# Optimization experiments

Measured on AMD Instinct MI355X. Metric: run time of the kernel, lower is better.

Reference implementation:

```python
import jax, jax.numpy as jnp
import numpy as np

N_NODES = 100_000
N_EDGES = 3_200_000


def setup_inputs() -> dict:
    key = jax.random.key(0)
    k = jax.random.split(key, 7)
    x = jax.random.normal(k[0], (N_NODES, 1), dtype=jnp.float32)
    edge_index = jax.random.randint(k[1], (2, N_EDGES), 0, N_NODES, dtype=jnp.int64)
    edge_weight = jax.random.uniform(k[2], (N_EDGES,), dtype=jnp.float32)
    # GCNConv params (glorot-style scale)
    W1 = jax.random.normal(k[3], (1, 16), dtype=jnp.float32) * 0.5
    b1 = jnp.zeros((16,), dtype=jnp.float32)
    W2 = jax.random.normal(k[4], (16, 2), dtype=jnp.float32) * 0.25
    b2 = jnp.zeros((2,), dtype=jnp.float32)
    return {"x": x, "edge_index": edge_index, "edge_weight": edge_weight,
            "W1": W1, "b1": b1, "W2": W2, "b2": b2}


def reference(x, edge_index, edge_weight, W1, b1, W2, b2):
    N = x.shape[0]
    src, dst = edge_index[0], edge_index[1]
    # GCN normalization with self-loops (fill value 1.0), cached across both layers
    loop = jnp.arange(N, dtype=edge_index.dtype)
    src_f = jnp.concatenate([src, loop])            # [E+N]
    dst_f = jnp.concatenate([dst, loop])            # [E+N]
    w_f = jnp.concatenate([edge_weight, jnp.ones((N,), dtype=edge_weight.dtype)])
    deg = jax.ops.segment_sum(w_f, dst_f, num_segments=N)   # [N]
    dinv = jnp.where(deg > 0, jax.lax.rsqrt(deg), 0.0)
    norm = dinv[src_f] * w_f * dinv[dst_f]          # [E+N]

    def gcn_layer(h, W, b):
        h = h @ W                                   # [N, F_out]
        msg = norm[:, None] * h[src_f]              # gather + weight  [E+N, F_out]
        agg = jax.ops.segment_sum(msg, dst_f, num_segments=N)  # scatter-add [N, F_out]
        return agg + b

    h = jax.nn.relu(gcn_layer(x, W1, b1))
    # F.dropout(training=self.training): identity at inference (reference is eval mode)
    out = gcn_layer(h, W2, b2)
    return jax.nn.log_softmax(out, axis=1)
```

## Files before the change

### kernel.cpp

```cpp
#include <hip/hip_runtime.h>
#include <math.h>


static constexpr int BLOCK_S   = 512;
static constexpr int EPB       = 4096;
static constexpr int VITERS    = EPB / (BLOCK_S * 4);
static constexpr int CHUNK     = 128;
static constexpr int LOG_CHUNK = 7;
static constexpr int BLOCK_A   = 512;
static constexpr int MAXNB     = 1024;
static constexpr int MAXBLK    = 1024;
static constexpr int TABCAP    = 5120;

__device__ __forceinline__ unsigned int incl_scan512(unsigned int v,
                                                     unsigned int* wsum, int t) {
    unsigned int x = v;
#pragma unroll
    for (int off = 1; off < 64; off <<= 1) {
        unsigned int y = __shfl_up(x, off, 64);
        if ((t & 63) >= off) x += y;
    }
    if ((t & 63) == 63) wsum[t >> 6] = x;
    __syncthreads();
    if (t < 8) {
        unsigned int s = wsum[t];
#pragma unroll
        for (int off = 1; off < 8; off <<= 1) {
            unsigned int y = __shfl_up(s, off, 64);
            if (t >= off) s += y;
        }
        wsum[t] = s;
    }
    __syncthreads();
    return x + ((t >= 64) ? wsum[(t >> 6) - 1] : 0u);
}

__device__ __forceinline__ int run_adj_fallback(const unsigned int* cumx,
                                                const int* radj,
                                                unsigned int i, int nblk) {
    int lo = 0, hi = nblk - 1;
    while (lo < hi) {
        int mid = (lo + hi + 1) >> 1;
        if (cumx[mid] <= i) lo = mid; else hi = mid - 1;
    }
    return radj[lo];
}


__global__ __launch_bounds__(BLOCK_S) void scatter_kernel(
    const int* __restrict__ src, const int* __restrict__ dst,
    const float* __restrict__ w,
    unsigned int* __restrict__ rowOffT,
    unsigned long long* __restrict__ payload,
    int E, int nb, int nblk) {
    __shared__ unsigned long long pbuf[EPB];
    __shared__ unsigned int hist[MAXNB];
    __shared__ unsigned int wsum[8];
    const int blk  = blockIdx.x;
    const int base = blk * EPB;
    const int nE   = min(EPB, E - base);
    const int t    = threadIdx.x;

    hist[t]           = 0u;
    hist[t + BLOCK_S] = 0u;
    __syncthreads();

    int4 dc[VITERS];
#pragma unroll
    for (int i = 0; i < VITERS; ++i) {
        const int k = 4 * t + i * 4 * BLOCK_S;
        int4 d4 = make_int4(0, 0, 0, 0);
        if (k < nE) {
            d4 = *reinterpret_cast<const int4*>(&dst[base + k]);
            atomicAdd(&hist[(unsigned int)d4.x >> LOG_CHUNK], 1u);
            atomicAdd(&hist[(unsigned int)d4.y >> LOG_CHUNK], 1u);
            atomicAdd(&hist[(unsigned int)d4.z >> LOG_CHUNK], 1u);
            atomicAdd(&hist[(unsigned int)d4.w >> LOG_CHUNK], 1u);
        }
        dc[i] = d4;
    }
    __syncthreads();

    const unsigned int v0 = hist[2 * t], v1 = hist[2 * t + 1];
    const unsigned int pr = v0 + v1;
    const unsigned int inclp = incl_scan512(pr, wsum, t);
    const unsigned int ex0 = inclp - pr;
    const unsigned int ex1 = ex0 + v0;
    if (2 * t < nb)     rowOffT[(size_t)(2 * t) * nblk + blk]     = ex0;
    if (2 * t + 1 < nb) rowOffT[(size_t)(2 * t + 1) * nblk + blk] = ex1;
    if (t == 0)         rowOffT[(size_t)nb * nblk + blk] = (unsigned int)nE;
    hist[2 * t]     = ex0;
    hist[2 * t + 1] = ex1;
    __syncthreads();

#pragma unroll
    for (int i = 0; i < VITERS; ++i) {
        const int k = 4 * t + i * 4 * BLOCK_S;
        if (k < nE) {
            const int4   d4 = dc[i];
            const int4   s4 = *reinterpret_cast<const int4*>(&src[base + k]);
            const float4 w4 = *reinterpret_cast<const float4*>(&w[base + k]);
#define SCAT_ONE(dd, ss, ww)                                                  \
            {                                                                 \
                const unsigned int slot =                                     \
                    atomicAdd(&hist[(unsigned int)(dd) >> LOG_CHUNK], 1u);    \
                pbuf[slot] =                                                  \
                    ((unsigned long long)__float_as_uint(ww) << 32) |         \
                    ((unsigned int)(ss) << LOG_CHUNK) |                       \
                    (unsigned int)((dd) & (CHUNK - 1));                       \
            }
            SCAT_ONE(d4.x, s4.x, w4.x)
            SCAT_ONE(d4.y, s4.y, w4.y)
            SCAT_ONE(d4.z, s4.z, w4.z)
            SCAT_ONE(d4.w, s4.w, w4.w)
#undef SCAT_ONE
        }
    }
    __syncthreads();
    for (int k2 = t; k2 < (nE >> 1); k2 += BLOCK_S) {
        ulonglong2 v = *reinterpret_cast<const ulonglong2*>(&pbuf[2 * k2]);
        *reinterpret_cast<ulonglong2*>(&payload[(size_t)base + 2 * k2]) = v;
    }
}


#define AGG_PROLOGUE                                                          \
    const int b = blockIdx.x, t = threadIdx.x;                                \
    const int e0 = 2 * t, e1 = 2 * t + 1;                                     \
    unsigned int s00 = 0, s01 = 0, len0 = 0, len1 = 0;                        \
    if (e0 < nblk) {                                                          \
        const uint2 r0 =                                                      \
            *reinterpret_cast<const uint2*>(&rowOffT[(size_t)b * nblk + e0]); \
        const uint2 r1 =                                                      \
            *reinterpret_cast<const uint2*>(&rowOffT[(size_t)(b + 1) * nblk + e0]); \
        s00 = r0.x; s01 = r0.y;                                               \
        len0 = r1.x - r0.x;                                                   \
        len1 = (e1 < nblk) ? (r1.y - r0.y) : 0u;                              \
    }                                                                         \
    const unsigned int pr_    = len0 + len1;                                  \
    const unsigned int inclp_ = incl_scan512(pr_, wsum, t);                   \
    const unsigned int ex0_   = inclp_ - pr_;                                 \
    const unsigned int ex1_   = ex0_ + len0;                                  \
    if (e0 < nblk) { cumx[e0] = ex0_; radj[e0] = (int)s00 - (int)ex0_ + e0 * EPB; } \
    if (e1 < nblk) { cumx[e1] = ex1_; radj[e1] = (int)s01 - (int)ex1_ + e1 * EPB; } \
    if (t == ((nblk - 1) >> 1)) totsh = inclp_;                               \
    if (t < CHUNK) acc[t] = 0.0f;                                             \
    __syncthreads();                                                          \
    const unsigned int total = totsh;                                         \
    for (int r = e0; r <= e1 && r < nblk; ++r) {                              \
        const unsigned int beg = cumx[r];                                     \
        const unsigned int end = (r == nblk - 1) ? total : cumx[r + 1];       \
        const unsigned int lim = min(end, (unsigned int)TABCAP);              \
        const int a_ = radj[r];                                               \
        for (unsigned int i = beg; i < lim; ++i) table[i] = a_;               \
    }                                                                         \
    __syncthreads();

#define TAB(i) (((i) < (unsigned int)TABCAP) ? table[i]                       \
                                             : run_adj_fallback(cumx, radj, (i), nblk))

__global__ __launch_bounds__(BLOCK_A) void deg_dinv_kernel(
    const unsigned long long* __restrict__ payload,
    const unsigned int* __restrict__ rowOffT,
    const float* __restrict__ x,
    float* __restrict__ dinv, float* __restrict__ xd,
    int N, int nb, int nblk) {
    __shared__ unsigned int cumx[MAXBLK];
    __shared__ int          radj[MAXBLK];
    __shared__ float        acc[CHUNK];
    __shared__ int          table[TABCAP];
    __shared__ unsigned int wsum[8];
    __shared__ unsigned int totsh;
    AGG_PROLOGUE
    unsigned int i = t;
    for (; i + 3u * BLOCK_A < total; i += 4u * BLOCK_A) {
        const unsigned int i0 = i, i1 = i + BLOCK_A, i2 = i + 2u * BLOCK_A,
                           i3 = i + 3u * BLOCK_A;
        const int a0 = TAB(i0), a1 = TAB(i1), a2 = TAB(i2), a3 = TAB(i3);
        const unsigned long long p0 = payload[(unsigned int)(a0 + (int)i0)];
        const unsigned long long p1 = payload[(unsigned int)(a1 + (int)i1)];
        const unsigned long long p2 = payload[(unsigned int)(a2 + (int)i2)];
        const unsigned long long p3 = payload[(unsigned int)(a3 + (int)i3)];
        atomicAdd(&acc[(unsigned int)p0 & (CHUNK - 1)],
                  __uint_as_float((unsigned int)(p0 >> 32)));
        atomicAdd(&acc[(unsigned int)p1 & (CHUNK - 1)],
                  __uint_as_float((unsigned int)(p1 >> 32)));
        atomicAdd(&acc[(unsigned int)p2 & (CHUNK - 1)],
                  __uint_as_float((unsigned int)(p2 >> 32)));
        atomicAdd(&acc[(unsigned int)p3 & (CHUNK - 1)],
                  __uint_as_float((unsigned int)(p3 >> 32)));
    }
    for (; i < total; i += BLOCK_A) {
        const int adj = TAB(i);
        const unsigned long long p = payload[(unsigned int)(adj + (int)i)];
        atomicAdd(&acc[(unsigned int)p & (CHUNK - 1)],
                  __uint_as_float((unsigned int)(p >> 32)));
    }
    __syncthreads();
    const int n = b * CHUNK + t;
    if (t < CHUNK && n < N) {
        const float d = acc[t] + 1.0f;
        const float r = (d > 0.0f) ? rsqrtf(d) : 0.0f;
        dinv[n] = r;
        xd[n]   = r * x[n];
    }
}

__global__ __launch_bounds__(BLOCK_A) void s_gamma_kernel(
    const unsigned long long* __restrict__ payload,
    const unsigned int* __restrict__ rowOffT,
    const float* __restrict__ dinv,
    const float* __restrict__ xd,
    const float* __restrict__ W1,
    const float* __restrict__ b1,
    const float* __restrict__ W2,
    float* __restrict__ gd, int N, int nb, int nblk) {
    __shared__ unsigned int cumx[MAXBLK];
    __shared__ int          radj[MAXBLK];
    __shared__ float        acc[CHUNK];
    __shared__ int          table[TABCAP];
    __shared__ unsigned int wsum[8];
    __shared__ unsigned int totsh;
    AGG_PROLOGUE
    unsigned int i = t;
    for (; i + 3u * BLOCK_A < total; i += 4u * BLOCK_A) {
        const unsigned int i0 = i, i1 = i + BLOCK_A, i2 = i + 2u * BLOCK_A,
                           i3 = i + 3u * BLOCK_A;
        const int a0 = TAB(i0), a1 = TAB(i1), a2 = TAB(i2), a3 = TAB(i3);
        const unsigned long long p0 = payload[(unsigned int)(a0 + (int)i0)];
        const unsigned long long p1 = payload[(unsigned int)(a1 + (int)i1)];
        const unsigned long long p2 = payload[(unsigned int)(a2 + (int)i2)];
        const unsigned long long p3 = payload[(unsigned int)(a3 + (int)i3)];
        const float f0 = xd[(int)(((unsigned int)p0) >> LOG_CHUNK)];
        const float f1 = xd[(int)(((unsigned int)p1) >> LOG_CHUNK)];
        const float f2 = xd[(int)(((unsigned int)p2) >> LOG_CHUNK)];
        const float f3 = xd[(int)(((unsigned int)p3) >> LOG_CHUNK)];
        atomicAdd(&acc[(unsigned int)p0 & (CHUNK - 1)],
                  __uint_as_float((unsigned int)(p0 >> 32)) * f0);
        atomicAdd(&acc[(unsigned int)p1 & (CHUNK - 1)],
                  __uint_as_float((unsigned int)(p1 >> 32)) * f1);
        atomicAdd(&acc[(unsigned int)p2 & (CHUNK - 1)],
                  __uint_as_float((unsigned int)(p2 >> 32)) * f2);
        atomicAdd(&acc[(unsigned int)p3 & (CHUNK - 1)],
                  __uint_as_float((unsigned int)(p3 >> 32)) * f3);
    }
    for (; i < total; i += BLOCK_A) {
        const int adj = TAB(i);
        const unsigned long long p = payload[(unsigned int)(adj + (int)i)];
        atomicAdd(&acc[(unsigned int)p & (CHUNK - 1)],
                  __uint_as_float((unsigned int)(p >> 32)) *
                      xd[(int)(((unsigned int)p) >> LOG_CHUNK)]);
    }
    __syncthreads();
    const int n = b * CHUNK + t;
    if (t < CHUNK && n < N) {
        const float dv = dinv[n];
        const float sv = dv * (acc[t] + xd[n]);
        float g = 0.0f;
#pragma unroll
        for (int f = 0; f < 16; ++f) {
            const float h = fmaxf(sv * W1[f] + b1[f], 0.0f);
            g += h * (W2[2 * f + 1] - W2[2 * f + 0]);
        }
        gd[n] = dv * g;
    }
}

__global__ __launch_bounds__(BLOCK_A) void d_out_kernel(
    const unsigned long long* __restrict__ payload,
    const unsigned int* __restrict__ rowOffT,
    const float* __restrict__ dinv,
    const float* __restrict__ gd,
    const float* __restrict__ b2,
    float* __restrict__ out, int N, int nb, int nblk) {
    __shared__ unsigned int cumx[MAXBLK];
    __shared__ int          radj[MAXBLK];
    __shared__ float        acc[CHUNK];
    __shared__ int          table[TABCAP];
    __shared__ unsigned int wsum[8];
    __shared__ unsigned int totsh;
    AGG_PROLOGUE
    unsigned int i = t;
    for (; i + 3u * BLOCK_A < total; i += 4u * BLOCK_A) {
        const unsigned int i0 = i, i1 = i + BLOCK_A, i2 = i + 2u * BLOCK_A,
                           i3 = i + 3u * BLOCK_A;
        const int a0 = TAB(i0), a1 = TAB(i1), a2 = TAB(i2), a3 = TAB(i3);
        const unsigned long long p0 = payload[(unsigned int)(a0 + (int)i0)];
        const unsigned long long p1 = payload[(unsigned int)(a1 + (int)i1)];
        const unsigned long long p2 = payload[(unsigned int)(a2 + (int)i2)];
        const unsigned long long p3 = payload[(unsigned int)(a3 + (int)i3)];
        const float f0 = gd[(int)(((unsigned int)p0) >> LOG_CHUNK)];
        const float f1 = gd[(int)(((unsigned int)p1) >> LOG_CHUNK)];
        const float f2 = gd[(int)(((unsigned int)p2) >> LOG_CHUNK)];
        const float f3 = gd[(int)(((unsigned int)p3) >> LOG_CHUNK)];
        atomicAdd(&acc[(unsigned int)p0 & (CHUNK - 1)],
                  __uint_as_float((unsigned int)(p0 >> 32)) * f0);
        atomicAdd(&acc[(unsigned int)p1 & (CHUNK - 1)],
                  __uint_as_float((unsigned int)(p1 >> 32)) * f1);
        atomicAdd(&acc[(unsigned int)p2 & (CHUNK - 1)],
                  __uint_as_float((unsigned int)(p2 >> 32)) * f2);
        atomicAdd(&acc[(unsigned int)p3 & (CHUNK - 1)],
                  __uint_as_float((unsigned int)(p3 >> 32)) * f3);
    }
    for (; i < total; i += BLOCK_A) {
        const int adj = TAB(i);
        const unsigned long long p = payload[(unsigned int)(adj + (int)i)];
        atomicAdd(&acc[(unsigned int)p & (CHUNK - 1)],
                  __uint_as_float((unsigned int)(p >> 32)) *
                      gd[(int)(((unsigned int)p) >> LOG_CHUNK)]);
    }
    __syncthreads();
    const int n = b * CHUNK + t;
    if (t < CHUNK && n < N) {
        const float dv = dinv[n];
        const float d = dv * (acc[t] + gd[n]) + (b2[1] - b2[0]);
        const float lse = fmaxf(d, 0.0f) + log1pf(expf(-fabsf(d)));
        out[2 * n + 0] = -lse;
        out[2 * n + 1] = d - lse;
    }
}


static constexpr int BLOCK = 256;

__global__ void zero_kernel(float* __restrict__ a, float* __restrict__ b, int n2) {
    int i = blockIdx.x * blockDim.x + threadIdx.x;
    if (i < n2) { a[i] = 0.0f; b[i] = 0.0f; }
}
__global__ void deg_kernel(const int* __restrict__ dst, const float* __restrict__ w,
                           float* __restrict__ deg, int E) {
    int e = blockIdx.x * blockDim.x + threadIdx.x;
    if (e < E) atomicAdd(&deg[dst[e]], w[e]);
}
__global__ void dinv_kernel(float* __restrict__ deg, int N) {
    int n = blockIdx.x * blockDim.x + threadIdx.x;
    if (n < N) {
        float d = deg[n] + 1.0f;
        deg[n] = (d > 0.0f) ? rsqrtf(d) : 0.0f;
    }
}
__global__ void s_kernel(const int* __restrict__ src, const int* __restrict__ dst,
                         const float* __restrict__ w, const float* __restrict__ dinv,
                         const float* __restrict__ x, float* __restrict__ s, int E) {
    int e = blockIdx.x * blockDim.x + threadIdx.x;
    if (e < E) {
        int si = src[e], di = dst[e];
        atomicAdd(&s[di], dinv[si] * w[e] * dinv[di] * x[si]);
    }
}
__global__ void g_kernel(const float* __restrict__ s, const float* __restrict__ dinv,
                         const float* __restrict__ x, const float* __restrict__ W1,
                         const float* __restrict__ b1, const float* __restrict__ W2,
                         float2* __restrict__ g, int N) {
    int n = blockIdx.x * blockDim.x + threadIdx.x;
    if (n < N) {
        float dv = dinv[n];
        float sv = s[n] + dv * dv * x[n];
        float g0 = 0.0f, g1 = 0.0f;
#pragma unroll
        for (int f = 0; f < 16; ++f) {
            float h = fmaxf(sv * W1[f] + b1[f], 0.0f);
            g0 += h * W2[2 * f + 0];
            g1 += h * W2[2 * f + 1];
        }
        g[n] = make_float2(g0, g1);
    }
}
__global__ void agg2_kernel(const int* __restrict__ src, const int* __restrict__ dst,
                            const float* __restrict__ w, const float* __restrict__ dinv,
                            const float2* __restrict__ g, float* __restrict__ agg, int E) {
    int e = blockIdx.x * blockDim.x + threadIdx.x;
    if (e < E) {
        int si = src[e], di = dst[e];
        float norm = dinv[si] * w[e] * dinv[di];
        float2 gv = g[si];
        atomicAdd(&agg[2 * di + 0], norm * gv.x);
        atomicAdd(&agg[2 * di + 1], norm * gv.y);
    }
}
__global__ void out_kernel(float* __restrict__ out, const float* __restrict__ dinv,
                           const float2* __restrict__ g, const float* __restrict__ b2, int N) {
    int n = blockIdx.x * blockDim.x + threadIdx.x;
    if (n < N) {
        float dv2 = dinv[n] * dinv[n];
        float2 gv = g[n];
        float a0 = out[2 * n + 0] + dv2 * gv.x + b2[0];
        float a1 = out[2 * n + 1] + dv2 * gv.y + b2[1];
        float m = fmaxf(a0, a1);
        float lse = m + logf(expf(a0 - m) + expf(a1 - m));
        out[2 * n + 0] = a0 - lse;
        out[2 * n + 1] = a1 - lse;
    }
}


extern "C" void kernel_launch(void* const* d_in, const int* in_sizes, int n_in,
                              void* d_out, int out_size, void* d_ws, size_t ws_size,
                              hipStream_t stream) {
    const float* x  = (const float*)d_in[0];
    const int*   ei = (const int*)d_in[1];
    const float* w  = (const float*)d_in[2];
    const float* W1 = (const float*)d_in[3];
    const float* b1 = (const float*)d_in[4];
    const float* W2 = (const float*)d_in[5];
    const float* b2 = (const float*)d_in[6];
    float* out = (float*)d_out;

    const int N = in_sizes[0];
    const int E = in_sizes[2];
    const int* src = ei;
    const int* dst = ei + E;

    const int nb   = (N + CHUNK - 1) / CHUNK;
    const int nblk = (E + EPB - 1) / EPB;

    size_t off = 0;
    size_t payload_off = off;  off += (size_t)nblk * EPB * 8;
    size_t rowoff_off  = off;  off += (size_t)(nb + 1) * nblk * 4 + 8;
    off = (off + 7) & ~(size_t)7;
    size_t dinv_off    = off;  off += (size_t)N * 4;
    size_t xd_off      = off;  off += (size_t)N * 4;
    size_t gd_off      = off;  off += (size_t)N * 4;
    const size_t required = off;

    const bool fits = (nb <= MAXNB && nb <= 2 * BLOCK_S && nblk <= MAXBLK &&
                       nblk <= 2 * BLOCK_A && (nblk & 1) == 0 && (E % 4) == 0 &&
                       ws_size >= required);

    if (fits) {
        char* wsb = (char*)d_ws;
        unsigned long long* payload = (unsigned long long*)(wsb + payload_off);
        unsigned int* rowOffT = (unsigned int*)(wsb + rowoff_off);
        float* dinv = (float*)(wsb + dinv_off);
        float* xd   = (float*)(wsb + xd_off);
        float* gd   = (float*)(wsb + gd_off);

        scatter_kernel <<<nblk, BLOCK_S, 0, stream>>>(src, dst, w, rowOffT, payload,
                                                      E, nb, nblk);
        deg_dinv_kernel<<<nb, BLOCK_A, 0, stream>>>(payload, rowOffT, x,
                                                    dinv, xd, N, nb, nblk);
        s_gamma_kernel <<<nb, BLOCK_A, 0, stream>>>(payload, rowOffT, dinv, xd,
                                                    W1, b1, W2, gd, N, nb, nblk);
        d_out_kernel   <<<nb, BLOCK_A, 0, stream>>>(payload, rowOffT, dinv, gd, b2,
                                                    out, N, nb, nblk);
    } else {
        float*  ws   = (float*)d_ws;
        float*  dinv = ws;
        float*  s    = ws + (size_t)N;
        float2* g    = (float2*)(ws + (size_t)2 * N);
        const int gridE  = (E + BLOCK - 1) / BLOCK;
        const int gridN  = (N + BLOCK - 1) / BLOCK;
        const int gridN2 = (2 * N + BLOCK - 1) / BLOCK;
        zero_kernel<<<gridN2, BLOCK, 0, stream>>>(ws, out, 2 * N);
        deg_kernel <<<gridE,  BLOCK, 0, stream>>>(dst, w, dinv, E);
        dinv_kernel<<<gridN,  BLOCK, 0, stream>>>(dinv, N);
        s_kernel   <<<gridE,  BLOCK, 0, stream>>>(src, dst, w, dinv, x, s, E);
        g_kernel   <<<gridN,  BLOCK, 0, stream>>>(s, dinv, x, W1, b1, W2, g, N);
        agg2_kernel<<<gridE,  BLOCK, 0, stream>>>(src, dst, w, dinv, g, out, E);
        out_kernel <<<gridN,  BLOCK, 0, stream>>>(out, dinv, g, b2, N);
    }
}
```

Before: 188.5 us.

## Compact per-bucket edge payload in degree pass for contiguous reuse in later aggregations

The degree kernel now copies each bucket's edge records, which it already reads from the segmented payload, into a contiguous padded per-bucket buffer and records the bucket count. The two later aggregation kernels read that compact buffer with 16-byte vector loads. This skips their run-offset scan, table build and indirect segmented addressing. Buckets larger than the pad size fall back to the old path through a sentinel count. The trade-off is an extra write of the payload in the first pass and more workspace memory.

```diff
diff --git a/kernel.cpp b/kernel.cpp
--- a/kernel.cpp
+++ b/kernel.cpp
@@ -11,6 +11,8 @@
 static constexpr int MAXNB     = 1024;
 static constexpr int MAXBLK    = 1024;
 static constexpr int TABCAP    = 5120;
+static constexpr int PAD       = 5120;
+static constexpr unsigned int SENT = 0xFFFFFFFFu;
 
 __device__ __forceinline__ unsigned int incl_scan512(unsigned int v,
                                                      unsigned int* wsum, int t) {
@@ -125,34 +127,34 @@
 
 
 #define AGG_PROLOGUE                                                          \
-    const int b = blockIdx.x, t = threadIdx.x;                                \
-    const int e0 = 2 * t, e1 = 2 * t + 1;                                     \
     unsigned int s00 = 0, s01 = 0, len0 = 0, len1 = 0;                        \
-    if (e0 < nblk) {                                                          \
-        const uint2 r0 =                                                      \
-            *reinterpret_cast<const uint2*>(&rowOffT[(size_t)b * nblk + e0]); \
-        const uint2 r1 =                                                      \
-            *reinterpret_cast<const uint2*>(&rowOffT[(size_t)(b + 1) * nblk + e0]); \
-        s00 = r0.x; s01 = r0.y;                                               \
-        len0 = r1.x - r0.x;                                                   \
-        len1 = (e1 < nblk) ? (r1.y - r0.y) : 0u;                              \
-    }                                                                         \
-    const unsigned int pr_    = len0 + len1;                                  \
-    const unsigned int inclp_ = incl_scan512(pr_, wsum, t);                   \
-    const unsigned int ex0_   = inclp_ - pr_;                                 \
-    const unsigned int ex1_   = ex0_ + len0;                                  \
-    if (e0 < nblk) { cumx[e0] = ex0_; radj[e0] = (int)s00 - (int)ex0_ + e0 * EPB; } \
-    if (e1 < nblk) { cumx[e1] = ex1_; radj[e1] = (int)s01 - (int)ex1_ + e1 * EPB; } \
-    if (t == ((nblk - 1) >> 1)) totsh = inclp_;                               \
-    if (t < CHUNK) acc[t] = 0.0f;                                             \
-    __syncthreads();                                                          \
-    const unsigned int total = totsh;                                         \
-    for (int r = e0; r <= e1 && r < nblk; ++r) {                              \
-        const unsigned int beg = cumx[r];                                     \
-        const unsigned int end = (r == nblk - 1) ? total : cumx[r + 1];       \
-        const unsigned int lim = min(end, (unsigned int)TABCAP);              \
-        const int a_ = radj[r];                                               \
-        for (unsigned int i = beg; i < lim; ++i) table[i] = a_;               \
+    {                                                                         \
+        const int e0 = 2 * t, e1 = 2 * t + 1;                                 \
+        if (e0 < nblk) {                                                      \
+            const uint2 r0 =                                                  \
+                *reinterpret_cast<const uint2*>(&rowOffT[(size_t)b * nblk + e0]); \
+            const uint2 r1 =                                                  \
+                *reinterpret_cast<const uint2*>(&rowOffT[(size_t)(b + 1) * nblk + e0]); \
+            s00 = r0.x; s01 = r0.y;                                           \
+            len0 = r1.x - r0.x;                                               \
+            len1 = (e1 < nblk) ? (r1.y - r0.y) : 0u;                          \
+        }                                                                     \
+        const unsigned int pr_    = len0 + len1;                              \
+        const unsigned int inclp_ = incl_scan512(pr_, wsum, t);               \
+        const unsigned int ex0_   = inclp_ - pr_;                             \
+        const unsigned int ex1_   = ex0_ + len0;                              \
+        if (e0 < nblk) { cumx[e0] = ex0_; radj[e0] = (int)s00 - (int)ex0_ + e0 * EPB; } \
+        if (e1 < nblk) { cumx[e1] = ex1_; radj[e1] = (int)s01 - (int)ex1_ + e1 * EPB; } \
+        if (t == ((nblk - 1) >> 1)) totsh = inclp_;                           \
+        __syncthreads();                                                      \
+        const unsigned int total_ = totsh;                                    \
+        for (int r = e0; r <= e1 && r < nblk; ++r) {                          \
+            const unsigned int beg = cumx[r];                                 \
+            const unsigned int end = (r == nblk - 1) ? total_ : cumx[r + 1];  \
+            const unsigned int lim = min(end, (unsigned int)TABCAP);          \
+            const int a_ = radj[r];                                           \
+            for (unsigned int i = beg; i < lim; ++i) table[i] = a_;           \
+        }                                                                     \
     }                                                                         \
     __syncthreads();
 
@@ -161,6 +163,8 @@
 
 __global__ __launch_bounds__(BLOCK_A) void deg_dinv_kernel(
     const unsigned long long* __restrict__ payload,
+    unsigned long long* __restrict__ payload2,
+    unsigned int* __restrict__ bucketCnt,
     const unsigned int* __restrict__ rowOffT,
     const float* __restrict__ x,
     float* __restrict__ dinv, float* __restrict__ xd,
@@ -171,7 +175,13 @@
     __shared__ int          table[TABCAP];
     __shared__ unsigned int wsum[8];
     __shared__ unsigned int totsh;
+    const int b = blockIdx.x, t = threadIdx.x;
+    if (t < CHUNK) acc[t] = 0.0f;
     AGG_PROLOGUE
+    const unsigned int total = totsh;
+    const bool canw = (total <= (unsigned int)PAD);
+    if (t == 0) bucketCnt[b] = canw ? total : SENT;
+    unsigned long long* const p2 = payload2 + (size_t)b * PAD;
     unsigned int i = t;
     for (; i + 3u * BLOCK_A < total; i += 4u * BLOCK_A) {
         const unsigned int i0 = i, i1 = i + BLOCK_A, i2 = i + 2u * BLOCK_A,
@@ -179,20 +189,24 @@
         const int a0 = TAB(i0), a1 = TAB(i1), a2 = TAB(i2), a3 = TAB(i3);
         const unsigned long long p0 = payload[(unsigned int)(a0 + (int)i0)];
         const unsigned long long p1 = payload[(unsigned int)(a1 + (int)i1)];
-        const unsigned long long p2 = payload[(unsigned int)(a2 + (int)i2)];
+        const unsigned long long p2v = payload[(unsigned int)(a2 + (int)i2)];
         const unsigned long long p3 = payload[(unsigned int)(a3 + (int)i3)];
+        if (canw) {
+            p2[i0] = p0; p2[i1] = p1; p2[i2] = p2v; p2[i3] = p3;
+        }
         atomicAdd(&acc[(unsigned int)p0 & (CHUNK - 1)],
                   __uint_as_float((unsigned int)(p0 >> 32)));
         atomicAdd(&acc[(unsigned int)p1 & (CHUNK - 1)],
                   __uint_as_float((unsigned int)(p1 >> 32)));
-        atomicAdd(&acc[(unsigned int)p2 & (CHUNK - 1)],
-                  __uint_as_float((unsigned int)(p2 >> 32)));
+        atomicAdd(&acc[(unsigned int)p2v & (CHUNK - 1)],
+                  __uint_as_float((unsigned int)(p2v >> 32)));
         atomicAdd(&acc[(unsigned int)p3 & (CHUNK - 1)],
                   __uint_as_float((unsigned int)(p3 >> 32)));
     }
     for (; i < total; i += BLOCK_A) {
         const int adj = TAB(i);
         const unsigned long long p = payload[(unsigned int)(adj + (int)i)];
+        if (canw) p2[i] = p;
         atomicAdd(&acc[(unsigned int)p & (CHUNK - 1)],
                   __uint_as_float((unsigned int)(p >> 32)));
     }
@@ -206,8 +220,62 @@
     }
 }
 
+
+#define FAST_BODY(GATHER_ARR)                                                 \
+    const size_t gbase = (size_t)b * PAD;                                     \
+    const unsigned int npair = cnt >> 1;                                      \
+    unsigned int j = t;                                                       \
+    for (; j + 3u * BLOCK_A < npair; j += 4u * BLOCK_A) {                     \
+        const ulonglong2 q0 = *reinterpret_cast<const ulonglong2*>(&payload2[gbase + 2u * j]); \
+        const ulonglong2 q1 = *reinterpret_cast<const ulonglong2*>(&payload2[gbase + 2u * (j + BLOCK_A)]); \
+        const ulonglong2 q2 = *reinterpret_cast<const ulonglong2*>(&payload2[gbase + 2u * (j + 2u * BLOCK_A)]); \
+        const ulonglong2 q3 = *reinterpret_cast<const ulonglong2*>(&payload2[gbase + 2u * (j + 3u * BLOCK_A)]); \
+        const float f0a = GATHER_ARR[(int)(((unsigned int)q0.x) >> LOG_CHUNK)]; \
+        const float f0b = GATHER_ARR[(int)(((unsigned int)q0.y) >> LOG_CHUNK)]; \
+        const float f1a = GATHER_ARR[(int)(((unsigned int)q1.x) >> LOG_CHUNK)]; \
+        const float f1b = GATHER_ARR[(int)(((unsigned int)q1.y) >> LOG_CHUNK)]; \
+        const float f2a = GATHER_ARR[(int)(((unsigned int)q2.x) >> LOG_CHUNK)]; \
+        const float f2b = GATHER_ARR[(int)(((unsigned int)q2.y) >> LOG_CHUNK)]; \
+        const float f3a = GATHER_ARR[(int)(((unsigned int)q3.x) >> LOG_CHUNK)]; \
+        const float f3b = GATHER_ARR[(int)(((unsigned int)q3.y) >> LOG_CHUNK)]; \
+        atomicAdd(&acc[(unsigned int)q0.x & (CHUNK - 1)], __uint_as_float((unsigned int)(q0.x >> 32)) * f0a); \
+        atomicAdd(&acc[(unsigned int)q0.y & (CHUNK - 1)], __uint_as_float((unsigned int)(q0.y >> 32)) * f0b); \
+        atomicAdd(&acc[(unsigned int)q1.x & (CHUNK - 1)], __uint_as_float((unsigned int)(q1.x >> 32)) * f1a); \
+        atomicAdd(&acc[(unsigned int)q1.y & (CHUNK - 1)], __uint_as_float((unsigned int)(q1.y >> 32)) * f1b); \
+        atomicAdd(&acc[(unsigned int)q2.x & (CHUNK - 1)], __uint_as_float((unsigned int)(q2.x >> 32)) * f2a); \
+        atomicAdd(&acc[(unsigned int)q2.y & (CHUNK - 1)], __uint_as_float((unsigned int)(q2.y >> 32)) * f2b); \
+        atomicAdd(&acc[(unsigned int)q3.x & (CHUNK - 1)], __uint_as_float((unsigned int)(q3.x >> 32)) * f3a); \
+        atomicAdd(&acc[(unsigned int)q3.y & (CHUNK - 1)], __uint_as_float((unsigned int)(q3.y >> 32)) * f3b); \
+    }                                                                         \
+    for (; j < npair; j += BLOCK_A) {                                         \
+        const ulonglong2 q = *reinterpret_cast<const ulonglong2*>(&payload2[gbase + 2u * j]); \
+        const float fa = GATHER_ARR[(int)(((unsigned int)q.x) >> LOG_CHUNK)]; \
+        const float fb = GATHER_ARR[(int)(((unsigned int)q.y) >> LOG_CHUNK)]; \
+        atomicAdd(&acc[(unsigned int)q.x & (CHUNK - 1)], __uint_as_float((unsigned int)(q.x >> 32)) * fa); \
+        atomicAdd(&acc[(unsigned int)q.y & (CHUNK - 1)], __uint_as_float((unsigned int)(q.y >> 32)) * fb); \
+    }                                                                         \
+    if ((cnt & 1u) && t == 0) {                                               \
+        const unsigned long long q = payload2[gbase + cnt - 1u];              \
+        atomicAdd(&acc[(unsigned int)q & (CHUNK - 1)],                        \
+                  __uint_as_float((unsigned int)(q >> 32)) *                  \
+                      GATHER_ARR[(int)(((unsigned int)q) >> LOG_CHUNK)]);     \
+    }
+
+#define FB_BODY(GATHER_ARR)                                                   \
+    AGG_PROLOGUE                                                              \
+    const unsigned int total = totsh;                                         \
+    for (unsigned int i = t; i < total; i += BLOCK_A) {                       \
+        const int adj = TAB(i);                                               \
+        const unsigned long long p = payload[(unsigned int)(adj + (int)i)];   \
+        atomicAdd(&acc[(unsigned int)p & (CHUNK - 1)],                        \
+                  __uint_as_float((unsigned int)(p >> 32)) *                  \
+                      GATHER_ARR[(int)(((unsigned int)p) >> LOG_CHUNK)]);     \
+    }
+
 __global__ __launch_bounds__(BLOCK_A) void s_gamma_kernel(
     const unsigned long long* __restrict__ payload,
+    const unsigned long long* __restrict__ payload2,
+    const unsigned int* __restrict__ bucketCnt,
     const unsigned int* __restrict__ rowOffT,
     const float* __restrict__ dinv,
     const float* __restrict__ xd,
@@ -221,35 +289,14 @@
     __shared__ int          table[TABCAP];
     __shared__ unsigned int wsum[8];
     __shared__ unsigned int totsh;
-    AGG_PROLOGUE
-    unsigned int i = t;
-    for (; i + 3u * BLOCK_A < total; i += 4u * BLOCK_A) {
-        const unsigned int i0 = i, i1 = i + BLOCK_A, i2 = i + 2u * BLOCK_A,
-                           i3 = i + 3u * BLOCK_A;
-        const int a0 = TAB(i0), a1 = TAB(i1), a2 = TAB(i2), a3 = TAB(i3);
-        const unsigned long long p0 = payload[(unsigned int)(a0 + (int)i0)];
-        const unsigned long long p1 = payload[(unsigned int)(a1 + (int)i1)];
-        const unsigned long long p2 = payload[(unsigned int)(a2 + (int)i2)];
-        const unsigned long long p3 = payload[(unsigned int)(a3 + (int)i3)];
-        const float f0 = xd[(int)(((unsigned int)p0) >> LOG_CHUNK)];
-        const float f1 = xd[(int)(((unsigned int)p1) >> LOG_CHUNK)];
-        const float f2 = xd[(int)(((unsigned int)p2) >> LOG_CHUNK)];
-        const float f3 = xd[(int)(((unsigned int)p3) >> LOG_CHUNK)];
-        atomicAdd(&acc[(unsigned int)p0 & (CHUNK - 1)],
-                  __uint_as_float((unsigned int)(p0 >> 32)) * f0);
-        atomicAdd(&acc[(unsigned int)p1 & (CHUNK - 1)],
-                  __uint_as_float((unsigned int)(p1 >> 32)) * f1);
-        atomicAdd(&acc[(unsigned int)p2 & (CHUNK - 1)],
-                  __uint_as_float((unsigned int)(p2 >> 32)) * f2);
-        atomicAdd(&acc[(unsigned int)p3 & (CHUNK - 1)],
-                  __uint_as_float((unsigned int)(p3 >> 32)) * f3);
-    }
-    for (; i < total; i += BLOCK_A) {
-        const int adj = TAB(i);
-        const unsigned long long p = payload[(unsigned int)(adj + (int)i)];
-        atomicAdd(&acc[(unsigned int)p & (CHUNK - 1)],
-                  __uint_as_float((unsigned int)(p >> 32)) *
-                      xd[(int)(((unsigned int)p) >> LOG_CHUNK)]);
+    const int b = blockIdx.x, t = threadIdx.x;
+    const unsigned int cnt = bucketCnt[b];
+    if (t < CHUNK) acc[t] = 0.0f;
+    __syncthreads();
+    if (cnt != SENT) {
+        FAST_BODY(xd)
+    } else {
+        FB_BODY(xd)
     }
     __syncthreads();
     const int n = b * CHUNK + t;
@@ -268,6 +315,8 @@
 
 __global__ __launch_bounds__(BLOCK_A) void d_out_kernel(
     const unsigned long long* __restrict__ payload,
+    const unsigned long long* __restrict__ payload2,
+    const unsigned int* __restrict__ bucketCnt,
     const unsigned int* __restrict__ rowOffT,
     const float* __restrict__ dinv,
     const float* __restrict__ gd,
@@ -279,35 +328,14 @@
     __shared__ int          table[TABCAP];
     __shared__ unsigned int wsum[8];
     __shared__ unsigned int totsh;
-    AGG_PROLOGUE
-    unsigned int i = t;
-    for (; i + 3u * BLOCK_A < total; i += 4u * BLOCK_A) {
-        const unsigned int i0 = i, i1 = i + BLOCK_A, i2 = i + 2u * BLOCK_A,
-                           i3 = i + 3u * BLOCK_A;
-        const int a0 = TAB(i0), a1 = TAB(i1), a2 = TAB(i2), a3 = TAB(i3);
-        const unsigned long long p0 = payload[(unsigned int)(a0 + (int)i0)];
-        const unsigned long long p1 = payload[(unsigned int)(a1 + (int)i1)];
-        const unsigned long long p2 = payload[(unsigned int)(a2 + (int)i2)];
-        const unsigned long long p3 = payload[(unsigned int)(a3 + (int)i3)];
-        const float f0 = gd[(int)(((unsigned int)p0) >> LOG_CHUNK)];
-        const float f1 = gd[(int)(((unsigned int)p1) >> LOG_CHUNK)];
-        const float f2 = gd[(int)(((unsigned int)p2) >> LOG_CHUNK)];
-        const float f3 = gd[(int)(((unsigned int)p3) >> LOG_CHUNK)];
-        atomicAdd(&acc[(unsigned int)p0 & (CHUNK - 1)],
-                  __uint_as_float((unsigned int)(p0 >> 32)) * f0);
-        atomicAdd(&acc[(unsigned int)p1 & (CHUNK - 1)],
-                  __uint_as_float((unsigned int)(p1 >> 32)) * f1);
-        atomicAdd(&acc[(unsigned int)p2 & (CHUNK - 1)],
-                  __uint_as_float((unsigned int)(p2 >> 32)) * f2);
-        atomicAdd(&acc[(unsigned int)p3 & (CHUNK - 1)],
-                  __uint_as_float((unsigned int)(p3 >> 32)) * f3);
-    }
-    for (; i < total; i += BLOCK_A) {
-        const int adj = TAB(i);
-        const unsigned long long p = payload[(unsigned int)(adj + (int)i)];
-        atomicAdd(&acc[(unsigned int)p & (CHUNK - 1)],
-                  __uint_as_float((unsigned int)(p >> 32)) *
-                      gd[(int)(((unsigned int)p) >> LOG_CHUNK)]);
+    const int b = blockIdx.x, t = threadIdx.x;
+    const unsigned int cnt = bucketCnt[b];
+    if (t < CHUNK) acc[t] = 0.0f;
+    __syncthreads();
+    if (cnt != SENT) {
+        FAST_BODY(gd)
+    } else {
+        FB_BODY(gd)
     }
     __syncthreads();
     const int n = b * CHUNK + t;
@@ -415,12 +443,14 @@
     const int nblk = (E + EPB - 1) / EPB;
 
     size_t off = 0;
-    size_t payload_off = off;  off += (size_t)nblk * EPB * 8;
-    size_t rowoff_off  = off;  off += (size_t)(nb + 1) * nblk * 4 + 8;
+    size_t payload_off  = off;  off += (size_t)nblk * EPB * 8;
+    size_t payload2_off = off;  off += (size_t)nb * PAD * 8;
+    size_t rowoff_off   = off;  off += (size_t)(nb + 1) * nblk * 4 + 8;
     off = (off + 7) & ~(size_t)7;
-    size_t dinv_off    = off;  off += (size_t)N * 4;
-    size_t xd_off      = off;  off += (size_t)N * 4;
-    size_t gd_off      = off;  off += (size_t)N * 4;
+    size_t bcnt_off     = off;  off += (size_t)nb * 4;
+    size_t dinv_off     = off;  off += (size_t)N * 4;
+    size_t xd_off       = off;  off += (size_t)N * 4;
+    size_t gd_off       = off;  off += (size_t)N * 4;
     const size_t required = off;
 
     const bool fits = (nb <= MAXNB && nb <= 2 * BLOCK_S && nblk <= MAXBLK &&
@@ -429,19 +459,23 @@
 
     if (fits) {
         char* wsb = (char*)d_ws;
-        unsigned long long* payload = (unsigned long long*)(wsb + payload_off);
-        unsigned int* rowOffT = (unsigned int*)(wsb + rowoff_off);
+        unsigned long long* payload  = (unsigned long long*)(wsb + payload_off);
+        unsigned long long* payload2 = (unsigned long long*)(wsb + payload2_off);
+        unsigned int* rowOffT   = (unsigned int*)(wsb + rowoff_off);
+        unsigned int* bucketCnt = (unsigned int*)(wsb + bcnt_off);
         float* dinv = (float*)(wsb + dinv_off);
         float* xd   = (float*)(wsb + xd_off);
         float* gd   = (float*)(wsb + gd_off);
 
         scatter_kernel <<<nblk, BLOCK_S, 0, stream>>>(src, dst, w, rowOffT, payload,
                                                       E, nb, nblk);
-        deg_dinv_kernel<<<nb, BLOCK_A, 0, stream>>>(payload, rowOffT, x,
-                                                    dinv, xd, N, nb, nblk);
-        s_gamma_kernel <<<nb, BLOCK_A, 0, stream>>>(payload, rowOffT, dinv, xd,
+        deg_dinv_kernel<<<nb, BLOCK_A, 0, stream>>>(payload, payload2, bucketCnt,
+                                                    rowOffT, x, dinv, xd, N, nb, nblk);
+        s_gamma_kernel <<<nb, BLOCK_A, 0, stream>>>(payload, payload2, bucketCnt,
+                                                    rowOffT, dinv, xd,
                                                     W1, b1, W2, gd, N, nb, nblk);
-        d_out_kernel   <<<nb, BLOCK_A, 0, stream>>>(payload, rowOffT, dinv, gd, b2,
+        d_out_kernel   <<<nb, BLOCK_A, 0, stream>>>(payload, payload2, bucketCnt,
+                                                    rowOffT, dinv, gd, b2,
                                                     out, N, nb, nblk);
     } else {
         float*  ws   = (float*)d_ws;
```

Result: faster. 182.8 us (-3.0%).

## Build globally bucket-contiguous payload via histogram and scan passes before scatter

Applied to the files above, without the earlier changes.

Replaces the per-block bucketed payload, which each aggregation kernel had to locate through a per-block offset table and lookup, with a global counting-sort layout. New hist, rowscan and bucket-scan kernels compute global bucket offsets, and the scatter kernel writes each edge straight to its final position. The three aggregation kernels then read one contiguous range per bucket and drop the scan and table prologue. In exchange, dst is read twice, three extra launches are added, and the final scatter writes to global memory are no longer coalesced.

```diff
diff --git a/kernel.cpp b/kernel.cpp
--- a/kernel.cpp
+++ b/kernel.cpp
@@ -10,7 +10,6 @@
 static constexpr int BLOCK_A   = 512;
 static constexpr int MAXNB     = 1024;
 static constexpr int MAXBLK    = 1024;
-static constexpr int TABCAP    = 5120;
 
 __device__ __forceinline__ unsigned int incl_scan512(unsigned int v,
                                                      unsigned int* wsum, int t) {
@@ -35,26 +34,84 @@
     return x + ((t >= 64) ? wsum[(t >> 6) - 1] : 0u);
 }
 
-__device__ __forceinline__ int run_adj_fallback(const unsigned int* cumx,
-                                                const int* radj,
-                                                unsigned int i, int nblk) {
-    int lo = 0, hi = nblk - 1;
-    while (lo < hi) {
-        int mid = (lo + hi + 1) >> 1;
-        if (cumx[mid] <= i) lo = mid; else hi = mid - 1;
-    }
-    return radj[lo];
-}
-
-
-__global__ __launch_bounds__(BLOCK_S) void scatter_kernel(
+__global__ __launch_bounds__(BLOCK_S) void hist_kernel(
+    const int* __restrict__ dst,
+    unsigned int* __restrict__ histT,
+    int E, int nb, int nblk) {
+    __shared__ unsigned int hist[MAXNB];
+    const int blk  = blockIdx.x;
+    const int base = blk * EPB;
+    const int nE   = min(EPB, E - base);
+    const int t    = threadIdx.x;
+
+    hist[t]           = 0u;
+    hist[t + BLOCK_S] = 0u;
+    __syncthreads();
+
+#pragma unroll
+    for (int i = 0; i < VITERS; ++i) {
+        const int k = 4 * t + i * 4 * BLOCK_S;
+        if (k < nE) {
+            const int4 d4 = *reinterpret_cast<const int4*>(&dst[base + k]);
+            atomicAdd(&hist[(unsigned int)d4.x >> LOG_CHUNK], 1u);
+            atomicAdd(&hist[(unsigned int)d4.y >> LOG_CHUNK], 1u);
+            atomicAdd(&hist[(unsigned int)d4.z >> LOG_CHUNK], 1u);
+            atomicAdd(&hist[(unsigned int)d4.w >> LOG_CHUNK], 1u);
+        }
+    }
+    __syncthreads();
+    if (2 * t < nb)     histT[(size_t)(2 * t) * nblk + blk]     = hist[2 * t];
+    if (2 * t + 1 < nb) histT[(size_t)(2 * t + 1) * nblk + blk] = hist[2 * t + 1];
+}
+
+__global__ __launch_bounds__(BLOCK_S) void rowscan_kernel(
+    const unsigned int* __restrict__ histT,
+    unsigned int* __restrict__ prefT,
+    unsigned int* __restrict__ bucketTotal,
+    int nblk) {
+    __shared__ unsigned int wsum[8];
+    const int b = blockIdx.x, t = threadIdx.x;
+    const int e0 = 2 * t;
+    unsigned int v0 = 0, v1 = 0;
+    if (e0 < nblk) {
+        const uint2 r = *reinterpret_cast<const uint2*>(&histT[(size_t)b * nblk + e0]);
+        v0 = r.x; v1 = r.y;
+    }
+    const unsigned int incl = incl_scan512(v0 + v1, wsum, t);
+    const unsigned int ex0  = incl - v0 - v1;
+    const unsigned int ex1  = ex0 + v0;
+    if (e0 < nblk)
+        *reinterpret_cast<uint2*>(&prefT[(size_t)b * nblk + e0]) = make_uint2(ex0, ex1);
+    if (t == BLOCK_S - 1) bucketTotal[b] = incl;
+}
+
+__global__ __launch_bounds__(BLOCK_S) void bscan_kernel(
+    const unsigned int* __restrict__ bucketTotal,
+    unsigned int* __restrict__ bucketStart,
+    int nb) {
+    __shared__ unsigned int wsum[8];
+    const int t = threadIdx.x;
+    const unsigned int v0 = (2 * t < nb)     ? bucketTotal[2 * t]     : 0u;
+    const unsigned int v1 = (2 * t + 1 < nb) ? bucketTotal[2 * t + 1] : 0u;
+    const unsigned int incl = incl_scan512(v0 + v1, wsum, t);
+    const unsigned int ex0  = incl - v0 - v1;
+    const unsigned int ex1  = ex0 + v0;
+    if (2 * t < nb)     bucketStart[2 * t]     = ex0;
+    if (2 * t + 1 < nb) bucketStart[2 * t + 1] = ex1;
+    if (t == BLOCK_S - 1) bucketStart[nb] = incl;
+}
+
+__global__ __launch_bounds__(BLOCK_S) void scatter2_kernel(
     const int* __restrict__ src, const int* __restrict__ dst,
     const float* __restrict__ w,
-    unsigned int* __restrict__ rowOffT,
-    unsigned long long* __restrict__ payload,
+    const unsigned int* __restrict__ prefT,
+    const unsigned int* __restrict__ bucketStart,
+    unsigned long long* __restrict__ payload2,
     int E, int nb, int nblk) {
     __shared__ unsigned long long pbuf[EPB];
+    __shared__ unsigned int gaddrA[EPB];
     __shared__ unsigned int hist[MAXNB];
+    __shared__ int          adjp[MAXNB];
     __shared__ unsigned int wsum[8];
     const int blk  = blockIdx.x;
     const int base = blk * EPB;
@@ -82,13 +139,16 @@
     __syncthreads();
 
     const unsigned int v0 = hist[2 * t], v1 = hist[2 * t + 1];
-    const unsigned int pr = v0 + v1;
-    const unsigned int inclp = incl_scan512(pr, wsum, t);
-    const unsigned int ex0 = inclp - pr;
+    const unsigned int inclp = incl_scan512(v0 + v1, wsum, t);
+    const unsigned int ex0 = inclp - v0 - v1;
     const unsigned int ex1 = ex0 + v0;
-    if (2 * t < nb)     rowOffT[(size_t)(2 * t) * nblk + blk]     = ex0;
-    if (2 * t + 1 < nb) rowOffT[(size_t)(2 * t + 1) * nblk + blk] = ex1;
-    if (t == 0)         rowOffT[(size_t)nb * nblk + blk] = (unsigned int)nE;
+    if (2 * t < nb) {
+        const uint2 bs = *reinterpret_cast<const uint2*>(&bucketStart[2 * t]);
+        adjp[2 * t] = (int)(bs.x + prefT[(size_t)(2 * t) * nblk + blk]) - (int)ex0;
+        if (2 * t + 1 < nb)
+            adjp[2 * t + 1] =
+                (int)(bs.y + prefT[(size_t)(2 * t + 1) * nblk + blk]) - (int)ex1;
+    }
     hist[2 * t]     = ex0;
     hist[2 * t + 1] = ex1;
     __syncthreads();
@@ -102,12 +162,13 @@
             const float4 w4 = *reinterpret_cast<const float4*>(&w[base + k]);
 #define SCAT_ONE(dd, ss, ww)                                                  \
             {                                                                 \
-                const unsigned int slot =                                     \
-                    atomicAdd(&hist[(unsigned int)(dd) >> LOG_CHUNK], 1u);    \
+                const int bkt = (int)((unsigned int)(dd) >> LOG_CHUNK);       \
+                const unsigned int slot = atomicAdd(&hist[bkt], 1u);          \
                 pbuf[slot] =                                                  \
                     ((unsigned long long)__float_as_uint(ww) << 32) |         \
                     ((unsigned int)(ss) << LOG_CHUNK) |                       \
                     (unsigned int)((dd) & (CHUNK - 1));                       \
+                gaddrA[slot] = (unsigned int)(adjp[bkt] + (int)slot);         \
             }
             SCAT_ONE(d4.x, s4.x, w4.x)
             SCAT_ONE(d4.y, s4.y, w4.y)
@@ -117,70 +178,27 @@
         }
     }
     __syncthreads();
-    for (int k2 = t; k2 < (nE >> 1); k2 += BLOCK_S) {
-        ulonglong2 v = *reinterpret_cast<const ulonglong2*>(&pbuf[2 * k2]);
-        *reinterpret_cast<ulonglong2*>(&payload[(size_t)base + 2 * k2]) = v;
-    }
-}
-
-
-#define AGG_PROLOGUE                                                          \
-    const int b = blockIdx.x, t = threadIdx.x;                                \
-    const int e0 = 2 * t, e1 = 2 * t + 1;                                     \
-    unsigned int s00 = 0, s01 = 0, len0 = 0, len1 = 0;                        \
-    if (e0 < nblk) {                                                          \
-        const uint2 r0 =                                                      \
-            *reinterpret_cast<const uint2*>(&rowOffT[(size_t)b * nblk + e0]); \
-        const uint2 r1 =                                                      \
-            *reinterpret_cast<const uint2*>(&rowOffT[(size_t)(b + 1) * nblk + e0]); \
-        s00 = r0.x; s01 = r0.y;                                               \
-        len0 = r1.x - r0.x;                                                   \
-        len1 = (e1 < nblk) ? (r1.y - r0.y) : 0u;                              \
-    }                                                                         \
-    const unsigned int pr_    = len0 + len1;                                  \
-    const unsigned int inclp_ = incl_scan512(pr_, wsum, t);                   \
-    const unsigned int ex0_   = inclp_ - pr_;                                 \
-    const unsigned int ex1_   = ex0_ + len0;                                  \
-    if (e0 < nblk) { cumx[e0] = ex0_; radj[e0] = (int)s00 - (int)ex0_ + e0 * EPB; } \
-    if (e1 < nblk) { cumx[e1] = ex1_; radj[e1] = (int)s01 - (int)ex1_ + e1 * EPB; } \
-    if (t == ((nblk - 1) >> 1)) totsh = inclp_;                               \
-    if (t < CHUNK) acc[t] = 0.0f;                                             \
-    __syncthreads();                                                          \
-    const unsigned int total = totsh;                                         \
-    for (int r = e0; r <= e1 && r < nblk; ++r) {                              \
-        const unsigned int beg = cumx[r];                                     \
-        const unsigned int end = (r == nblk - 1) ? total : cumx[r + 1];       \
-        const unsigned int lim = min(end, (unsigned int)TABCAP);              \
-        const int a_ = radj[r];                                               \
-        for (unsigned int i = beg; i < lim; ++i) table[i] = a_;               \
-    }                                                                         \
-    __syncthreads();
-
-#define TAB(i) (((i) < (unsigned int)TABCAP) ? table[i]                       \
-                                             : run_adj_fallback(cumx, radj, (i), nblk))
-
-__global__ __launch_bounds__(BLOCK_A) void deg_dinv_kernel(
-    const unsigned long long* __restrict__ payload,
-    const unsigned int* __restrict__ rowOffT,
+    for (int k = t; k < nE; k += BLOCK_S)
+        payload2[gaddrA[k]] = pbuf[k];
+}
+
+__global__ __launch_bounds__(BLOCK_A) void deg2_kernel(
+    const unsigned long long* __restrict__ payload2,
+    const unsigned int* __restrict__ bucketStart,
     const float* __restrict__ x,
     float* __restrict__ dinv, float* __restrict__ xd,
-    int N, int nb, int nblk) {
-    __shared__ unsigned int cumx[MAXBLK];
-    __shared__ int          radj[MAXBLK];
-    __shared__ float        acc[CHUNK];
-    __shared__ int          table[TABCAP];
-    __shared__ unsigned int wsum[8];
-    __shared__ unsigned int totsh;
-    AGG_PROLOGUE
-    unsigned int i = t;
-    for (; i + 3u * BLOCK_A < total; i += 4u * BLOCK_A) {
-        const unsigned int i0 = i, i1 = i + BLOCK_A, i2 = i + 2u * BLOCK_A,
-                           i3 = i + 3u * BLOCK_A;
-        const int a0 = TAB(i0), a1 = TAB(i1), a2 = TAB(i2), a3 = TAB(i3);
-        const unsigned long long p0 = payload[(unsigned int)(a0 + (int)i0)];
-        const unsigned long long p1 = payload[(unsigned int)(a1 + (int)i1)];
-        const unsigned long long p2 = payload[(unsigned int)(a2 + (int)i2)];
-        const unsigned long long p3 = payload[(unsigned int)(a3 + (int)i3)];
+    int N, int nb) {
+    __shared__ float acc[CHUNK];
+    const int b = blockIdx.x, t = threadIdx.x;
+    if (t < CHUNK) acc[t] = 0.0f;
+    __syncthreads();
+    const unsigned int beg = bucketStart[b], end = bucketStart[b + 1];
+    unsigned int i = beg + t;
+    for (; i + 3u * BLOCK_A < end; i += 4u * BLOCK_A) {
+        const unsigned long long p0 = payload2[i];
+        const unsigned long long p1 = payload2[i + BLOCK_A];
+        const unsigned long long p2 = payload2[i + 2u * BLOCK_A];
+        const unsigned long long p3 = payload2[i + 3u * BLOCK_A];
         atomicAdd(&acc[(unsigned int)p0 & (CHUNK - 1)],
                   __uint_as_float((unsigned int)(p0 >> 32)));
         atomicAdd(&acc[(unsigned int)p1 & (CHUNK - 1)],
@@ -190,9 +208,8 @@
         atomicAdd(&acc[(unsigned int)p3 & (CHUNK - 1)],
                   __uint_as_float((unsigned int)(p3 >> 32)));
     }
-    for (; i < total; i += BLOCK_A) {
-        const int adj = TAB(i);
-        const unsigned long long p = payload[(unsigned int)(adj + (int)i)];
+    for (; i < end; i += BLOCK_A) {
+        const unsigned long long p = payload2[i];
         atomicAdd(&acc[(unsigned int)p & (CHUNK - 1)],
                   __uint_as_float((unsigned int)(p >> 32)));
     }
@@ -206,51 +223,48 @@
     }
 }
 
-__global__ __launch_bounds__(BLOCK_A) void s_gamma_kernel(
-    const unsigned long long* __restrict__ payload,
-    const unsigned int* __restrict__ rowOffT,
+#define AGG2_BODY(GATHER_ARR)                                                 \
+    const unsigned int beg = bucketStart[b], end = bucketStart[b + 1];        \
+    unsigned int i = beg + t;                                                 \
+    for (; i + 3u * BLOCK_A < end; i += 4u * BLOCK_A) {                       \
+        const unsigned long long p0 = payload2[i];                            \
+        const unsigned long long p1 = payload2[i + BLOCK_A];                  \
+        const unsigned long long p2 = payload2[i + 2u * BLOCK_A];             \
+        const unsigned long long p3 = payload2[i + 3u * BLOCK_A];             \
+        const float f0 = GATHER_ARR[(int)(((unsigned int)p0) >> LOG_CHUNK)];  \
+        const float f1 = GATHER_ARR[(int)(((unsigned int)p1) >> LOG_CHUNK)];  \
+        const float f2 = GATHER_ARR[(int)(((unsigned int)p2) >> LOG_CHUNK)];  \
+        const float f3 = GATHER_ARR[(int)(((unsigned int)p3) >> LOG_CHUNK)];  \
+        atomicAdd(&acc[(unsigned int)p0 & (CHUNK - 1)],                       \
+                  __uint_as_float((unsigned int)(p0 >> 32)) * f0);            \
+        atomicAdd(&acc[(unsigned int)p1 & (CHUNK - 1)],                       \
+                  __uint_as_float((unsigned int)(p1 >> 32)) * f1);            \
+        atomicAdd(&acc[(unsigned int)p2 & (CHUNK - 1)],                       \
+                  __uint_as_float((unsigned int)(p2 >> 32)) * f2);            \
+        atomicAdd(&acc[(unsigned int)p3 & (CHUNK - 1)],                       \
+                  __uint_as_float((unsigned int)(p3 >> 32)) * f3);            \
+    }                                                                         \
+    for (; i < end; i += BLOCK_A) {                                           \
+        const unsigned long long p = payload2[i];                             \
+        atomicAdd(&acc[(unsigned int)p & (CHUNK - 1)],                        \
+                  __uint_as_float((unsigned int)(p >> 32)) *                  \
+                      GATHER_ARR[(int)(((unsigned int)p) >> LOG_CHUNK)]);     \
+    }
+
+__global__ __launch_bounds__(BLOCK_A) void s_gamma2_kernel(
+    const unsigned long long* __restrict__ payload2,
+    const unsigned int* __restrict__ bucketStart,
     const float* __restrict__ dinv,
     const float* __restrict__ xd,
     const float* __restrict__ W1,
     const float* __restrict__ b1,
     const float* __restrict__ W2,
-    float* __restrict__ gd, int N, int nb, int nblk) {
-    __shared__ unsigned int cumx[MAXBLK];
-    __shared__ int          radj[MAXBLK];
-    __shared__ float        acc[CHUNK];
-    __shared__ int          table[TABCAP];
-    __shared__ unsigned int wsum[8];
-    __shared__ unsigned int totsh;
-    AGG_PROLOGUE
-    unsigned int i = t;
-    for (; i + 3u * BLOCK_A < total; i += 4u * BLOCK_A) {
-        const unsigned int i0 = i, i1 = i + BLOCK_A, i2 = i + 2u * BLOCK_A,
-                           i3 = i + 3u * BLOCK_A;
-        const int a0 = TAB(i0), a1 = TAB(i1), a2 = TAB(i2), a3 = TAB(i3);
-        const unsigned long long p0 = payload[(unsigned int)(a0 + (int)i0)];
-        const unsigned long long p1 = payload[(unsigned int)(a1 + (int)i1)];
-        const unsigned long long p2 = payload[(unsigned int)(a2 + (int)i2)];
-        const unsigned long long p3 = payload[(unsigned int)(a3 + (int)i3)];
-        const float f0 = xd[(int)(((unsigned int)p0) >> LOG_CHUNK)];
-        const float f1 = xd[(int)(((unsigned int)p1) >> LOG_CHUNK)];
-        const float f2 = xd[(int)(((unsigned int)p2) >> LOG_CHUNK)];
-        const float f3 = xd[(int)(((unsigned int)p3) >> LOG_CHUNK)];
-        atomicAdd(&acc[(unsigned int)p0 & (CHUNK - 1)],
-                  __uint_as_float((unsigned int)(p0 >> 32)) * f0);
-        atomicAdd(&acc[(unsigned int)p1 & (CHUNK - 1)],
-                  __uint_as_float((unsigned int)(p1 >> 32)) * f1);
-        atomicAdd(&acc[(unsigned int)p2 & (CHUNK - 1)],
-                  __uint_as_float((unsigned int)(p2 >> 32)) * f2);
-        atomicAdd(&acc[(unsigned int)p3 & (CHUNK - 1)],
-                  __uint_as_float((unsigned int)(p3 >> 32)) * f3);
-    }
-    for (; i < total; i += BLOCK_A) {
-        const int adj = TAB(i);
-        const unsigned long long p = payload[(unsigned int)(adj + (int)i)];
-        atomicAdd(&acc[(unsigned int)p & (CHUNK - 1)],
-                  __uint_as_float((unsigned int)(p >> 32)) *
-                      xd[(int)(((unsigned int)p) >> LOG_CHUNK)]);
-    }
+    float* __restrict__ gd, int N, int nb) {
+    __shared__ float acc[CHUNK];
+    const int b = blockIdx.x, t = threadIdx.x;
+    if (t < CHUNK) acc[t] = 0.0f;
+    __syncthreads();
+    AGG2_BODY(xd)
     __syncthreads();
     const int n = b * CHUNK + t;
     if (t < CHUNK && n < N) {
@@ -266,49 +280,18 @@
     }
 }
 
-__global__ __launch_bounds__(BLOCK_A) void d_out_kernel(
-    const unsigned long long* __restrict__ payload,
-    const unsigned int* __restrict__ rowOffT,
+__global__ __launch_bounds__(BLOCK_A) void d_out2_kernel(
+    const unsigned long long* __restrict__ payload2,
+    const unsigned int* __restrict__ bucketStart,
     const float* __restrict__ dinv,
     const float* __restrict__ gd,
     const float* __restrict__ b2,
-    float* __restrict__ out, int N, int nb, int nblk) {
-    __shared__ unsigned int cumx[MAXBLK];
-    __shared__ int          radj[MAXBLK];
-    __shared__ float        acc[CHUNK];
-    __shared__ int          table[TABCAP];
-    __shared__ unsigned int wsum[8];
-    __shared__ unsigned int totsh;
-    AGG_PROLOGUE
-    unsigned int i = t;
-    for (; i + 3u * BLOCK_A < total; i += 4u * BLOCK_A) {
-        const unsigned int i0 = i, i1 = i + BLOCK_A, i2 = i + 2u * BLOCK_A,
-                           i3 = i + 3u * BLOCK_A;
-        const int a0 = TAB(i0), a1 = TAB(i1), a2 = TAB(i2), a3 = TAB(i3);
-        const unsigned long long p0 = payload[(unsigned int)(a0 + (int)i0)];
-        const unsigned long long p1 = payload[(unsigned int)(a1 + (int)i1)];
-        const unsigned long long p2 = payload[(unsigned int)(a2 + (int)i2)];
-        const unsigned long long p3 = payload[(unsigned int)(a3 + (int)i3)];
-        const float f0 = gd[(int)(((unsigned int)p0) >> LOG_CHUNK)];
-        const float f1 = gd[(int)(((unsigned int)p1) >> LOG_CHUNK)];
-        const float f2 = gd[(int)(((unsigned int)p2) >> LOG_CHUNK)];
-        const float f3 = gd[(int)(((unsigned int)p3) >> LOG_CHUNK)];
-        atomicAdd(&acc[(unsigned int)p0 & (CHUNK - 1)],
-                  __uint_as_float((unsigned int)(p0 >> 32)) * f0);
-        atomicAdd(&acc[(unsigned int)p1 & (CHUNK - 1)],
-                  __uint_as_float((unsigned int)(p1 >> 32)) * f1);
-        atomicAdd(&acc[(unsigned int)p2 & (CHUNK - 1)],
-                  __uint_as_float((unsigned int)(p2 >> 32)) * f2);
-        atomicAdd(&acc[(unsigned int)p3 & (CHUNK - 1)],
-                  __uint_as_float((unsigned int)(p3 >> 32)) * f3);
-    }
-    for (; i < total; i += BLOCK_A) {
-        const int adj = TAB(i);
-        const unsigned long long p = payload[(unsigned int)(adj + (int)i)];
-        atomicAdd(&acc[(unsigned int)p & (CHUNK - 1)],
-                  __uint_as_float((unsigned int)(p >> 32)) *
-                      gd[(int)(((unsigned int)p) >> LOG_CHUNK)]);
-    }
+    float* __restrict__ out, int N, int nb) {
+    __shared__ float acc[CHUNK];
+    const int b = blockIdx.x, t = threadIdx.x;
+    if (t < CHUNK) acc[t] = 0.0f;
+    __syncthreads();
+    AGG2_BODY(gd)
     __syncthreads();
     const int n = b * CHUNK + t;
     if (t < CHUNK && n < N) {
@@ -415,34 +398,42 @@
     const int nblk = (E + EPB - 1) / EPB;
 
     size_t off = 0;
-    size_t payload_off = off;  off += (size_t)nblk * EPB * 8;
-    size_t rowoff_off  = off;  off += (size_t)(nb + 1) * nblk * 4 + 8;
-    off = (off + 7) & ~(size_t)7;
-    size_t dinv_off    = off;  off += (size_t)N * 4;
-    size_t xd_off      = off;  off += (size_t)N * 4;
-    size_t gd_off      = off;  off += (size_t)N * 4;
+    auto align16 = [](size_t v) { return (v + 15) & ~(size_t)15; };
+    size_t payload2_off = off;  off = align16(off + (size_t)E * 8);
+    size_t histT_off    = off;  off = align16(off + (size_t)nb * nblk * 4);
+    size_t prefT_off    = off;  off = align16(off + (size_t)nb * nblk * 4);
+    size_t btot_off     = off;  off = align16(off + (size_t)nb * 4);
+    size_t bstart_off   = off;  off = align16(off + (size_t)(nb + 1) * 4);
+    size_t dinv_off     = off;  off = align16(off + (size_t)N * 4);
+    size_t xd_off       = off;  off = align16(off + (size_t)N * 4);
+    size_t gd_off       = off;  off = align16(off + (size_t)N * 4);
     const size_t required = off;
 
-    const bool fits = (nb <= MAXNB && nb <= 2 * BLOCK_S && nblk <= MAXBLK &&
-                       nblk <= 2 * BLOCK_A && (nblk & 1) == 0 && (E % 4) == 0 &&
-                       ws_size >= required);
+    const bool fits = (nb <= MAXNB && nblk <= MAXBLK && (nblk & 1) == 0 &&
+                       (E % 4) == 0 && ws_size >= required);
 
     if (fits) {
         char* wsb = (char*)d_ws;
-        unsigned long long* payload = (unsigned long long*)(wsb + payload_off);
-        unsigned int* rowOffT = (unsigned int*)(wsb + rowoff_off);
+        unsigned long long* payload2 = (unsigned long long*)(wsb + payload2_off);
+        unsigned int* histT       = (unsigned int*)(wsb + histT_off);
+        unsigned int* prefT       = (unsigned int*)(wsb + prefT_off);
+        unsigned int* bucketTotal = (unsigned int*)(wsb + btot_off);
+        unsigned int* bucketStart = (unsigned int*)(wsb + bstart_off);
         float* dinv = (float*)(wsb + dinv_off);
         float* xd   = (float*)(wsb + xd_off);
         float* gd   = (float*)(wsb + gd_off);
 
-        scatter_kernel <<<nblk, BLOCK_S, 0, stream>>>(src, dst, w, rowOffT, payload,
-                                                      E, nb, nblk);
-        deg_dinv_kernel<<<nb, BLOCK_A, 0, stream>>>(payload, rowOffT, x,
-                                                    dinv, xd, N, nb, nblk);
-        s_gamma_kernel <<<nb, BLOCK_A, 0, stream>>>(payload, rowOffT, dinv, xd,
-                                                    W1, b1, W2, gd, N, nb, nblk);
-        d_out_kernel   <<<nb, BLOCK_A, 0, stream>>>(payload, rowOffT, dinv, gd, b2,
-                                                    out, N, nb, nblk);
+        hist_kernel    <<<nblk, BLOCK_S, 0, stream>>>(dst, histT, E, nb, nblk);
+        rowscan_kernel <<<nb,   BLOCK_S, 0, stream>>>(histT, prefT, bucketTotal, nblk);
+        bscan_kernel   <<<1,    BLOCK_S, 0, stream>>>(bucketTotal, bucketStart, nb);
+        scatter2_kernel<<<nblk, BLOCK_S, 0, stream>>>(src, dst, w, prefT, bucketStart,
+                                                      payload2, E, nb, nblk);
+        deg2_kernel    <<<nb,   BLOCK_A, 0, stream>>>(payload2, bucketStart, x,
+                                                      dinv, xd, N, nb);
+        s_gamma2_kernel<<<nb,   BLOCK_A, 0, stream>>>(payload2, bucketStart, dinv, xd,
+                                                      W1, b1, W2, gd, N, nb);
+        d_out2_kernel  <<<nb,   BLOCK_A, 0, stream>>>(payload2, bucketStart, dinv, gd,
+                                                      b2, out, N, nb);
     } else {
         float*  ws   = (float*)d_ws;
         float*  dinv = ws;
```

New measurement: 187.6 us. No clear change (-0.5%).
